# Kernel optimization log

Measured on AMD Instinct MI355X. Metric: run time of the kernel, lower is better.

The kernel has to match this reference:

```python
import jax, jax.numpy as jnp
import numpy as np

N_NODES = 20000
N_EDGES = 160000
FEAT = 512
HEADS = 4
NEG_SLOPE = 0.2


def setup_inputs() -> dict:
    key = jax.random.key(0)
    ks = jax.random.split(key, 8)
    s = 1.0 / np.sqrt(FEAT)
    return {
        "x": jax.random.normal(ks[0], (N_NODES, FEAT), dtype=jnp.float32),
        "edge_index": jax.random.randint(ks[1], (2, N_EDGES), 0, N_NODES, dtype=jnp.int32),
        "W_l": jax.random.normal(ks[2], (FEAT, HEADS * FEAT), dtype=jnp.float32) * s,
        "W_r": jax.random.normal(ks[3], (FEAT, HEADS * FEAT), dtype=jnp.float32) * s,
        "att": jax.random.normal(ks[4], (HEADS, FEAT), dtype=jnp.float32) * s,
        "bias": jax.random.normal(ks[5], (FEAT,), dtype=jnp.float32) * 0.01,
        "W_cls": jax.random.normal(ks[6], (FEAT, 2), dtype=jnp.float32) * s,
        "b_cls": jnp.zeros((2,), dtype=jnp.float32),
    }


def reference(x, edge_index, W_l, W_r, att, bias, W_cls, b_cls):
    N = x.shape[0]
    H, C = att.shape
    # PyG GATv2Conv default: add self-loops
    loops = jnp.arange(N, dtype=edge_index.dtype)
    ei = jnp.concatenate([edge_index, jnp.stack([loops, loops])], axis=1)
    src, dst = ei[0], ei[1]  # message j -> i

    xl = (x @ W_l).reshape(N, H, C)  # source transform
    xr = (x @ W_r).reshape(N, H, C)  # target transform

    # GATv2 score: e_ij = att . LeakyReLU(xl_j + xr_i)   -> [E, H]
    u = xl[src] + xr[dst]                      # [E, H, C]
    e = jnp.einsum('ehc,hc->eh', jax.nn.leaky_relu(u, NEG_SLOPE), att)

    # segment softmax over incoming edges of each dst node
    m = jax.ops.segment_max(e, dst, num_segments=N)          # [N, H]
    alpha = jnp.exp(e - m[dst])
    denom = jax.ops.segment_sum(alpha, dst, num_segments=N)  # [N, H]
    alpha = alpha / denom[dst]

    # aggregate: out_i = sum_j alpha_ij * xl_j
    out = jax.ops.segment_sum(alpha[:, :, None] * xl[src], dst, num_segments=N)  # [N,H,C]
    out = out.mean(axis=1) + bias  # concat=False -> mean over heads, then bias

    return out @ W_cls + b_cls  # [N, num_classes]
```

## Files before the change

### kernel.cpp

```cpp
#include <hip/hip_runtime.h>
#include <hip/hip_bf16.h>

#define FEAT    512
#define HEADS   4
#define NEG     0.2f

typedef unsigned int uint;
typedef unsigned short ushort_t;
typedef __attribute__((ext_vector_type(8))) short bf16x8v;
typedef __attribute__((ext_vector_type(4))) float f32x4v;
typedef __attribute__((ext_vector_type(4))) uint uint4v;
typedef __attribute__((address_space(3))) uint lds_u32_t;
typedef __attribute__((address_space(1))) const uint g_u32_t;

__device__ inline float bf2f(ushort_t h) { return __uint_as_float(((uint)h) << 16); }
__device__ inline ushort_t f2bf(float f) {
    uint u = __float_as_uint(f);
    u += 0x7fff + ((u >> 16) & 1);
    return (ushort_t)(u >> 16);
}
__device__ inline float2 up2(uint d) {
    return make_float2(__uint_as_float(d << 16), __uint_as_float(d & 0xffff0000u));
}
__device__ inline float2 f2add(float2 a, float2 b) { return make_float2(a.x + b.x, a.y + b.y); }
__device__ inline float2 f2min0(float2 a) { return make_float2(fminf(a.x, 0.f), fminf(a.y, 0.f)); }
__device__ inline float2 f2fma(float2 a, float2 b, float2 c) {
    return make_float2(fmaf(a.x, b.x, c.x), fmaf(a.y, b.y, c.y));
}
__device__ inline float2 f2fmas(float s, float2 b, float2 c) {
    return make_float2(fmaf(s, b.x, c.x), fmaf(s, b.y, c.y));
}

__global__ __launch_bounds__(256) void prep_kernel(
    const ushort_t* __restrict__ xprobe, int* flag,
    int* __restrict__ deg, int N, int NBZ,
    const void* a0, ushort_t* o0, int n0, const void* a1, ushort_t* o1, int n1,
    const void* a2, ushort_t* o2, int n2, const void* a3, ushort_t* o3, int n3,
    const void* __restrict__ Wl, const void* __restrict__ Wr,
    ushort_t* __restrict__ WtL, ushort_t* __restrict__ WtR, int Kk, int HCk, int nT,
    const void* __restrict__ xin, ushort_t* __restrict__ xc, long long nx) {
    __shared__ int s_isbf;
    __shared__ ushort_t t[64][72];
    int tid = threadIdx.x;
    if (tid < 64) {
        int hits = 0;
        for (int i = tid; i < 128; i += 64) {
            ushort_t w = xprobe[2 * i];
            uint hb = (w >> 8) & 0x7f;
            hits += (hb >= 0x38 && hb <= 0x42) ? 1 : 0;
        }
        #pragma unroll
        for (int off = 32; off >= 1; off >>= 1) hits += __shfl_xor(hits, off);
        if (tid == 0) s_isbf = (hits >= 64) ? 1 : 0;
    }
    __syncthreads();
    int isbf = s_isbf;
    int b = blockIdx.x;
    if (b == 0 && tid == 0) *flag = isbf;

    if (b < NBZ) {
        int i0 = (b * 256 + tid) * 4;
        if (i0 + 4 <= N) *(int4*)&deg[i0] = make_int4(0, 0, 0, 0);
        else for (int j = 0; j < 4; ++j) if (i0 + j < N) deg[i0 + j] = 0;
        return;
    }
    if (b < NBZ + 15) {
        int idx = (b - NBZ) * 256 + tid;
        const void* srcs[4] = {a0, a1, a2, a3};
        ushort_t* dsts[4] = {o0, o1, o2, o3};
        int ns[4] = {n0, n1, n2, n3};
        #pragma unroll
        for (int k = 0; k < 4; ++k) {
            if (idx < ns[k]) {
                dsts[k][idx] = isbf ? ((const ushort_t*)srcs[k])[idx]
                                    : f2bf(((const float*)srcs[k])[idx]);
                return;
            }
            idx -= ns[k];
        }
        return;
    }
    if (b < NBZ + 15 + nT) {
        int b2 = b - (NBZ + 15);
        int z = b2 & 1;
        int rest = b2 >> 1;
        int ntk = Kk >> 6;
        int ky = rest % ntk, nxt = rest / ntk;
        const void* in = z ? Wr : Wl;
        ushort_t* outp = z ? WtR : WtL;
        int k0 = ky * 64, n0 = nxt * 64;
        int r = tid >> 3;
        int c = (tid & 7) * 8;
        #pragma unroll
        for (int p = 0; p < 2; ++p) {
            int row = r + p * 32;
            size_t base = (size_t)(k0 + row) * HCk + n0 + c;
            if (isbf) {
                *(uint4*)&t[row][c] = *(const uint4*)((const ushort_t*)in + base);
            } else {
                const float* f = (const float*)in + base;
                float4 a = *(const float4*)f, bb = *(const float4*)(f + 4);
                ushort_t o[8] = {f2bf(a.x), f2bf(a.y), f2bf(a.z), f2bf(a.w),
                                 f2bf(bb.x), f2bf(bb.y), f2bf(bb.z), f2bf(bb.w)};
                *(uint4*)&t[row][c] = *(uint4*)o;
            }
        }
        __syncthreads();
        #pragma unroll
        for (int p = 0; p < 2; ++p) {
            int row = r + p * 32;
            #pragma unroll
            for (int j = 0; j < 8; ++j)
                outp[(size_t)(n0 + row) * Kk + k0 + c + j] = t[c + j][row];
        }
        return;
    }
    if (isbf) return;
    long long i0 = ((long long)(b - NBZ - 15 - nT) * 256 + tid) * 8;
    if (i0 + 8 <= nx) {
        const float* f = (const float*)xin + i0;
        float4 a = *(const float4*)f, bb = *(const float4*)(f + 4);
        ushort_t o[8] = {f2bf(a.x), f2bf(a.y), f2bf(a.z), f2bf(a.w),
                         f2bf(bb.x), f2bf(bb.y), f2bf(bb.z), f2bf(bb.w)};
        *(uint4*)&xc[i0] = *(uint4*)o;
    } else {
        for (long long i = i0; i < nx; ++i) xc[i] = f2bf(((const float*)xin)[i]);
    }
}

__global__ void hist_kernel(const int* __restrict__ dst, int* deg, int E, int N) {
    int i = blockIdx.x * blockDim.x + threadIdx.x;
    if (i < E) {
        int d = dst[i];
        if ((uint)d < (uint)N) atomicAdd(&deg[d], 1);
    }
}

__global__ __launch_bounds__(256) void scan1(const int* __restrict__ deg, int* __restrict__ part,
                                             int* __restrict__ bsum, int N) {
    __shared__ int tmp[256];
    int b = blockIdx.x, tid = threadIdx.x;
    int i0 = b * 1024 + tid * 4;
    int v[4] = {0, 0, 0, 0};
    if (i0 + 4 <= N) { int4 q = *(const int4*)&deg[i0]; v[0]=q.x+1; v[1]=q.y+1; v[2]=q.z+1; v[3]=q.w+1; }
    else { for (int j = 0; j < 4; ++j) v[j] = (i0 + j < N) ? deg[i0 + j] + 1 : 0; }
    int s0 = v[0], s1 = s0 + v[1], s2 = s1 + v[2], s3 = s2 + v[3];
    tmp[tid] = s3;
    __syncthreads();
    for (int off = 1; off < 256; off <<= 1) {
        int t = (tid >= off) ? tmp[tid - off] : 0;
        __syncthreads();
        tmp[tid] += t;
        __syncthreads();
    }
    int base = tid ? tmp[tid - 1] : 0;
    int e[4] = {base, base + s0, base + s1, base + s2};
    if (i0 + 4 <= N) { *(int4*)&part[i0] = make_int4(e[0], e[1], e[2], e[3]); }
    else { for (int j = 0; j < 4; ++j) if (i0 + j < N) part[i0 + j] = e[j]; }
    if (tid == 255) bsum[b] = tmp[255];
}

__global__ __launch_bounds__(256) void scan3(const int* __restrict__ part, const int* __restrict__ bsum,
                                             int* __restrict__ offsets, int* __restrict__ cursor,
                                             int N, int Nb) {
    __shared__ int s_add, s_tot;
    int b = blockIdx.x, tid = threadIdx.x;
    if (tid < 64) {
        int v = (tid < Nb) ? bsum[tid] : 0;
        int incl = v;
        #pragma unroll
        for (int off = 1; off < 64; off <<= 1) {
            int t = __shfl_up(incl, off);
            if (tid >= off) incl += t;
        }
        if (tid == b) s_add = incl - v;
        if (tid == Nb - 1) s_tot = incl;
    }
    __syncthreads();
    int add = s_add;
    int i0 = b * 1024 + tid * 4;
    #pragma unroll
    for (int j = 0; j < 4; ++j) {
        int i = i0 + j;
        if (i < N) { int o = part[i] + add; offsets[i] = o; cursor[i] = o; }
    }
    if (b == Nb - 1 && tid == 0) offsets[N] = s_tot;
}

__global__ void scatter_kernel(const int* __restrict__ src, const int* __restrict__ dst,
                               int* cursor, int* srcs, int E, int N) {
    int i = blockIdx.x * blockDim.x + threadIdx.x;
    if (i >= E + N) return;
    int s, d;
    if (i < E) { s = src[i]; d = dst[i]; }
    else       { s = i - E; d = i - E; }
    if ((uint)d >= (uint)N) return;
    int pos = atomicAdd(&cursor[d], 1);
    if ((uint)pos < (uint)(E + N)) srcs[pos] = s;
}

__global__ __launch_bounds__(256) void gemm128(const ushort_t* A_bf, const ushort_t* A_cv,
                                               const int* __restrict__ flag,
                                               const ushort_t* __restrict__ Bt,
                                               ushort_t* __restrict__ C,
                                               int M, int Nn, int K) {
    constexpr int CSTR = 132;
    __shared__ ushort_t SH[128 * CSTR];
    ushort_t* As = SH;
    ushort_t* Bs = SH + 8192;
    const ushort_t* A = (*flag) ? A_bf : A_cv;
    int tid = threadIdx.x;
    int wave = tid >> 6, lane = tid & 63;
    int row0 = blockIdx.y * 128, col0 = blockIdx.x * 128;
    int wm = (wave >> 1) * 64, wn = (wave & 1) * 64;

    f32x4v acc[4][4];
    #pragma unroll
    for (int i = 0; i < 4; ++i)
        #pragma unroll
        for (int j = 0; j < 4; ++j) acc[i][j] = (f32x4v){0.f, 0.f, 0.f, 0.f};

    int fm = lane & 15, kq8 = (lane >> 4) * 8;

    const ushort_t* srcA[2]; ushort_t* dstA0[2]; ushort_t* dstA1[2];
    const ushort_t* srcB[2]; ushort_t* dstB0[2]; ushort_t* dstB1[2];
    #pragma unroll
    for (int i = 0; i < 2; ++i) {
        int p = (wave * 2 + i) * 64 + lane;
        int row = p >> 2, kp = p & 3;
        int gra = row0 + row; if (gra >= M) gra = M - 1;
        srcA[i] = &A[(size_t)gra * K + kp * 8];
        srcB[i] = &Bt[(size_t)(col0 + row) * K + kp * 8];
        dstA0[i] = &As[p * 8]; dstA1[i] = &As[4096 + p * 8];
        dstB0[i] = &Bs[p * 8]; dstB1[i] = &Bs[4096 + p * 8];
    }

    for (int k0 = 0; k0 < K; k0 += 64) {
        #pragma unroll
        for (int i = 0; i < 2; ++i) {
            __builtin_amdgcn_global_load_lds((g_u32_t*)srcA[i],        (lds_u32_t*)dstA0[i], 16, 0, 0);
            __builtin_amdgcn_global_load_lds((g_u32_t*)(srcA[i] + 32), (lds_u32_t*)dstA1[i], 16, 0, 0);
            __builtin_amdgcn_global_load_lds((g_u32_t*)srcB[i],        (lds_u32_t*)dstB0[i], 16, 0, 0);
            __builtin_amdgcn_global_load_lds((g_u32_t*)(srcB[i] + 32), (lds_u32_t*)dstB1[i], 16, 0, 0);
            srcA[i] += 64; srcB[i] += 64;
        }
        __syncthreads();

        #pragma unroll
        for (int panel = 0; panel < 2; ++panel) {
            bf16x8v af[4], bfr[4];
            #pragma unroll
            for (int mi = 0; mi < 4; ++mi)
                af[mi] = *(const bf16x8v*)&As[panel * 4096 + (wm + mi * 16 + fm) * 32 + kq8];
            #pragma unroll
            for (int nj = 0; nj < 4; ++nj)
                bfr[nj] = *(const bf16x8v*)&Bs[panel * 4096 + (wn + nj * 16 + fm) * 32 + kq8];
            #pragma unroll
            for (int mi = 0; mi < 4; ++mi)
                #pragma unroll
                for (int nj = 0; nj < 4; ++nj)
                    acc[mi][nj] = __builtin_amdgcn_mfma_f32_16x16x32_bf16(af[mi], bfr[nj], acc[mi][nj], 0, 0, 0);
        }
        __syncthreads();
    }

    int col = lane & 15, rq = (lane >> 4) * 4;
    #pragma unroll
    for (int mi = 0; mi < 4; ++mi)
        #pragma unroll
        for (int r = 0; r < 4; ++r)
            #pragma unroll
            for (int nj = 0; nj < 4; ++nj)
                SH[(wm + mi * 16 + rq + r) * CSTR + wn + nj * 16 + col] = f2bf(acc[mi][nj][r]);
    __syncthreads();
    #pragma unroll
    for (int j = 0; j < 8; ++j) {
        int base = (tid + j * 256) * 8;
        int r = base >> 7, c = base & 127;
        int gm = row0 + r;
        if (gm < M)
            *(uint4*)&C[(size_t)gm * Nn + col0 + c] = *(const uint4*)&SH[r * CSTR + c];
    }
}

__global__ __launch_bounds__(128, 4) void gat_aggregate(
    const ushort_t* __restrict__ xl, int xl_stride,
    const ushort_t* __restrict__ xr, int xr_stride,
    const int* __restrict__ offsets, const int* __restrict__ srcs,
    const ushort_t* __restrict__ att, const ushort_t* __restrict__ bias,
    const ushort_t* __restrict__ Wc, const ushort_t* __restrict__ bc,
    float* __restrict__ out, int c0, int Cn, int N, int EN) {
    int bn = blockIdx.x;
    if (bn >= Cn) return;
    int n = c0 + bn;
    int tid = threadIdx.x;
    int w = tid >> 6, lane = tid & 63;
    int h = 2 * w + (lane >> 5);
    int r = lane & 31;
    int hoff = h * FEAT + r * 16;

    __shared__ float sh[HEADS][FEAT];
    __shared__ float r0s[2], r1s[2];

    float2 xrr[8], attr[8];
    { const uint4v* p = (const uint4v*)&xr[(size_t)bn * xr_stride + hoff];
      uint4v qa = __builtin_nontemporal_load(p);
      uint4v qb = __builtin_nontemporal_load(p + 1);
      xrr[0] = up2(qa.x); xrr[1] = up2(qa.y); xrr[2] = up2(qa.z); xrr[3] = up2(qa.w);
      xrr[4] = up2(qb.x); xrr[5] = up2(qb.y); xrr[6] = up2(qb.z); xrr[7] = up2(qb.w); }
    { const ushort_t* p = &att[hoff];
      uint4 qa = *(const uint4*)p, qb = *(const uint4*)(p + 8);
      attr[0] = up2(qa.x); attr[1] = up2(qa.y); attr[2] = up2(qa.z); attr[3] = up2(qa.w);
      attr[4] = up2(qb.x); attr[5] = up2(qb.y); attr[6] = up2(qb.z); attr[7] = up2(qb.w); }

    int start = offsets[n], end = offsets[n + 1];
    start = max(0, min(start, EN));
    end   = max(start, min(end, EN));
    int deg = end - start;

    int sv = 0;
    if (lane < deg) sv = srcs[start + lane];

    float l = 0.f;
    float2 acc[8] = {{0.f,0.f},{0.f,0.f},{0.f,0.f},{0.f,0.f},
                     {0.f,0.f},{0.f,0.f},{0.f,0.f},{0.f,0.f}};
    const ushort_t* xlh = xl + hoff;
    const float2 cneg = make_float2(NEG - 1.0f, NEG - 1.0f);

    auto getS = [&](int i) -> int {
        if (i >= deg) i = deg - 1;
        if (i < 0) i = 0;
        int s = (i < 64) ? __shfl(sv, i) : srcs[start + i];
        return ((uint)s >= (uint)N) ? 0 : s;
    };
    auto fetchE = [&](int i, uint4& qa, uint4& qb) {
        int s = getS(i);
        const ushort_t* pp = xlh + (size_t)s * xl_stride;
        qa = *(const uint4*)pp;
        qb = *(const uint4*)(pp + 8);
    };
    auto body = [&](uint4 qa, uint4 qb) {
        float2 v[8] = {up2(qa.x), up2(qa.y), up2(qa.z), up2(qa.w),
                       up2(qb.x), up2(qb.y), up2(qb.z), up2(qb.w)};
        float2 p2 = make_float2(0.f, 0.f);
        #pragma unroll
        for (int j = 0; j < 8; ++j) {
            float2 u  = f2add(v[j], xrr[j]);
            float2 lr = f2fma(f2min0(u), cneg, u);
            p2 = f2fma(lr, attr[j], p2);
        }
        float p = p2.x + p2.y;
        #pragma unroll
        for (int off = 16; off >= 1; off >>= 1) p += __shfl_xor(p, off);
        float wgt = __expf(p);
        l += wgt;
        #pragma unroll
        for (int j = 0; j < 8; ++j) acc[j] = f2fmas(wgt, v[j], acc[j]);
    };

    uint4 a0q, a0r, a1q, a1r, b0q, b0r, b1q, b1r;
    fetchE(0, a0q, a0r);
    fetchE(1, a1q, a1r);
    for (int e = 0; e < deg; e += 2) {
        fetchE(e + 2, b0q, b0r);
        fetchE(e + 3, b1q, b1r);
        body(a0q, a0r);
        if (e + 1 < deg) body(a1q, a1r);
        a0q = b0q; a0r = b0r; a1q = b1q; a1r = b1r;
    }

    float inv = 0.25f / fmaxf(l, 1e-35f);
    #pragma unroll
    for (int j = 0; j < 8; ++j) {
        sh[h][r * 16 + 2 * j]     = acc[j].x * inv;
        sh[h][r * 16 + 2 * j + 1] = acc[j].y * inv;
    }
    __syncthreads();

    float p0 = 0.f, p1 = 0.f;
    #pragma unroll
    for (int c = tid; c < FEAT; c += 128) {
        float f = sh[0][c] + sh[1][c] + sh[2][c] + sh[3][c] + bf2f(bias[c]);
        uint w2 = *(const uint*)&Wc[c * 2];
        p0 = fmaf(f, bf2f((ushort_t)(w2 & 0xffff)), p0);
        p1 = fmaf(f, bf2f((ushort_t)(w2 >> 16)), p1);
    }
    #pragma unroll
    for (int off = 32; off >= 1; off >>= 1) {
        p0 += __shfl_xor(p0, off);
        p1 += __shfl_xor(p1, off);
    }
    if (lane == 0) { r0s[w] = p0; r1s[w] = p1; }
    __syncthreads();
    if (tid == 0) {
        out[(size_t)n * 2 + 0] = r0s[0] + r0s[1] + bf2f(bc[0]);
        out[(size_t)n * 2 + 1] = r1s[0] + r1s[1] + bf2f(bc[1]);
    }
}

extern "C" void kernel_launch(void* const* d_in, const int* in_sizes, int n_in,
                              void* d_out, int out_size, void* d_ws, size_t ws_size,
                              hipStream_t stream) {
    const void* x    = d_in[0];
    const int*  ei   = (const int*)d_in[1];
    const void* W_l  = d_in[2];
    const void* W_r  = d_in[3];
    const void* att  = d_in[4];
    const void* bias = d_in[5];
    const void* Wc   = d_in[6];
    const void* bc   = d_in[7];
    float* out = (float*)d_out;

    const int N  = in_sizes[0] / FEAT;
    const int E  = in_sizes[1] / 2;
    const int K  = FEAT;
    const int HC = HEADS * FEAT;
    const int EN = E + N;
    const int Nb = (N + 1023) / 1024;

    const int* src = ei;
    const int* dst = ei + E;

    char* base = (char*)d_ws;
    size_t off = 0;
    auto alloc = [&](size_t bytes) -> char* {
        char* p = base + off;
        off = (off + bytes + 255) & ~(size_t)255;
        return p;
    };
    int* flag    = (int*)alloc(4);
    int* offsets = (int*)alloc((size_t)(N + 1) * 4);
    int* cursor  = (int*)alloc((size_t)N * 4);
    int* deg     = (int*)alloc((size_t)N * 4);
    int* part    = (int*)alloc((size_t)N * 4);
    int* bsum    = (int*)alloc((size_t)(Nb + 1) * 4);
    int* srcs    = (int*)alloc((size_t)EN * 4);
    ushort_t* attc  = (ushort_t*)alloc((size_t)HC * 2);
    ushort_t* biasc = (ushort_t*)alloc((size_t)FEAT * 2);
    ushort_t* Wcc   = (ushort_t*)alloc((size_t)FEAT * 2 * 2);
    ushort_t* bcc   = (ushort_t*)alloc(2 * 2);
    ushort_t* xc   = (ushort_t*)alloc((size_t)N * K * 2);
    ushort_t* Wcat = (ushort_t*)alloc((size_t)2 * HC * K * 2);
    size_t fixed = off;

    size_t need_merged = (size_t)N * 2 * HC * 2;
    bool merged = (ws_size >= fixed + need_merged);

    long long NX = (long long)N * K;
    const int NBZ = (N + 1023) / 1024;
    const int nT = (HC / 64) * (K / 64) * 2;
    int nxb = (int)((NX / 8 + 255) / 256);
    prep_kernel<<<NBZ + 15 + nT + nxb, 256, 0, stream>>>(
        (const ushort_t*)x, flag, deg, N, NBZ,
        att, attc, HC, bias, biasc, FEAT, Wc, Wcc, FEAT * 2, bc, bcc, 2,
        W_l, W_r, Wcat, Wcat + (size_t)HC * K, K, HC, nT,
        x, xc, NX);

    hist_kernel<<<(E + 255) / 256, 256, 0, stream>>>(dst, deg, E, N);
    scan1<<<Nb, 256, 0, stream>>>(deg, part, bsum, N);
    scan3<<<Nb, 256, 0, stream>>>(part, bsum, offsets, cursor, N, Nb);
    scatter_kernel<<<(EN + 255) / 256, 256, 0, stream>>>(src, dst, cursor, srcs, E, N);

    const ushort_t* x_bf = (const ushort_t*)x;

    if (merged) {
        ushort_t* xlr = (ushort_t*)(base + fixed);
        dim3 gg(2 * HC / 128, (N + 127) / 128);
        gemm128<<<gg, 256, 0, stream>>>(x_bf, xc, flag, Wcat, xlr, N, 2 * HC, K);
        gat_aggregate<<<N, 128, 0, stream>>>(xlr, 2 * HC, xlr + HC, 2 * HC,
                                             offsets, srcs, attc, biasc, Wcc, bcc,
                                             out, 0, N, N, EN);
    } else {
        ushort_t* xl = (ushort_t*)alloc((size_t)N * HC * 2);
        size_t remain = (ws_size > off) ? (ws_size - off) : 0;
        long long Cmax = (long long)(remain / ((size_t)HC * 2));
        int C = (Cmax >= N) ? N : (int)(Cmax & ~63LL);
        if (C < 64) C = 64;
        ushort_t* xrc = (ushort_t*)(base + off);
        ushort_t* Wlt = Wcat;
        ushort_t* Wrt = Wcat + (size_t)HC * K;

        dim3 gl(HC / 128, (N + 127) / 128);
        gemm128<<<gl, 256, 0, stream>>>(x_bf, xc, flag, Wlt, xl, N, HC, K);
        for (int c0 = 0; c0 < N; c0 += C) {
            int Cn = (N - c0 < C) ? (N - c0) : C;
            dim3 gr(HC / 128, (Cn + 127) / 128);
            gemm128<<<gr, 256, 0, stream>>>(x_bf + (size_t)c0 * K, xc + (size_t)c0 * K, flag,
                                            Wrt, xrc, Cn, HC, K);
            gat_aggregate<<<Cn, 128, 0, stream>>>(xl, HC, xrc, HC,
                                                  offsets, srcs, attc, biasc, Wcc, bcc,
                                                  out, c0, Cn, N, EN);
        }
    }
}
```

Before: 331.3 us.

## Fold histogram into x-convert kernel, scatter into GEMM grid, use packed f32 math

Moves the x fp32-to-bf16 conversion out of prep_kernel into a new kernel that also does the degree histogram, and drops the standalone hist_kernel launch. The CSR scatter now runs as extra blocks appended to the merged GEMM grid. The aim is fewer launches and letting the scatter overlap with GEMM work. The aggregation inner loop uses inline-asm v_pk_add_f32/v_pk_fma_f32 on float2 vectors to halve VALU instruction count. The risks are atomic contention alongside the GEMM blocks, and inline asm limiting compiler scheduling.

```diff
diff --git a/kernel.cpp b/kernel.cpp
--- a/kernel.cpp
+++ b/kernel.cpp
@@ -9,6 +9,7 @@
 typedef unsigned short ushort_t;
 typedef __attribute__((ext_vector_type(8))) short bf16x8v;
 typedef __attribute__((ext_vector_type(4))) float f32x4v;
+typedef __attribute__((ext_vector_type(2))) float f32x2v;
 typedef __attribute__((ext_vector_type(4))) uint uint4v;
 typedef __attribute__((address_space(3))) uint lds_u32_t;
 typedef __attribute__((address_space(1))) const uint g_u32_t;
@@ -19,16 +20,17 @@
     u += 0x7fff + ((u >> 16) & 1);
     return (ushort_t)(u >> 16);
 }
-__device__ inline float2 up2(uint d) {
-    return make_float2(__uint_as_float(d << 16), __uint_as_float(d & 0xffff0000u));
-}
-__device__ inline float2 f2add(float2 a, float2 b) { return make_float2(a.x + b.x, a.y + b.y); }
-__device__ inline float2 f2min0(float2 a) { return make_float2(fminf(a.x, 0.f), fminf(a.y, 0.f)); }
-__device__ inline float2 f2fma(float2 a, float2 b, float2 c) {
-    return make_float2(fmaf(a.x, b.x, c.x), fmaf(a.y, b.y, c.y));
-}
-__device__ inline float2 f2fmas(float s, float2 b, float2 c) {
-    return make_float2(fmaf(s, b.x, c.x), fmaf(s, b.y, c.y));
+__device__ inline f32x2v pk_add(f32x2v a, f32x2v b) {
+    f32x2v d; asm("v_pk_add_f32 %0, %1, %2" : "=v"(d) : "v"(a), "v"(b)); return d;
+}
+__device__ inline f32x2v pk_fma(f32x2v a, f32x2v b, f32x2v c) {
+    f32x2v d; asm("v_pk_fma_f32 %0, %1, %2, %3" : "=v"(d) : "v"(a), "v"(b), "v"(c)); return d;
+}
+__device__ inline f32x2v up2v(uint d) {
+    f32x2v r; r.x = __uint_as_float(d << 16); r.y = __uint_as_float(d & 0xffff0000u); return r;
+}
+__device__ inline f32x2v pk_min0(f32x2v a) {
+    f32x2v r; r.x = fminf(a.x, 0.f); r.y = fminf(a.y, 0.f); return r;
 }
 
 __global__ __launch_bounds__(256) void prep_kernel(
@@ -37,8 +39,7 @@
     const void* a0, ushort_t* o0, int n0, const void* a1, ushort_t* o1, int n1,
     const void* a2, ushort_t* o2, int n2, const void* a3, ushort_t* o3, int n3,
     const void* __restrict__ Wl, const void* __restrict__ Wr,
-    ushort_t* __restrict__ WtL, ushort_t* __restrict__ WtR, int Kk, int HCk, int nT,
-    const void* __restrict__ xin, ushort_t* __restrict__ xc, long long nx) {
+    ushort_t* __restrict__ WtL, ushort_t* __restrict__ WtR, int Kk, int HCk) {
     __shared__ int s_isbf;
     __shared__ ushort_t t[64][72];
     int tid = threadIdx.x;
@@ -80,43 +81,69 @@
         }
         return;
     }
-    if (b < NBZ + 15 + nT) {
-        int b2 = b - (NBZ + 15);
-        int z = b2 & 1;
-        int rest = b2 >> 1;
-        int ntk = Kk >> 6;
-        int ky = rest % ntk, nxt = rest / ntk;
-        const void* in = z ? Wr : Wl;
-        ushort_t* outp = z ? WtR : WtL;
-        int k0 = ky * 64, n0 = nxt * 64;
-        int r = tid >> 3;
-        int c = (tid & 7) * 8;
-        #pragma unroll
-        for (int p = 0; p < 2; ++p) {
-            int row = r + p * 32;
-            size_t base = (size_t)(k0 + row) * HCk + n0 + c;
-            if (isbf) {
-                *(uint4*)&t[row][c] = *(const uint4*)((const ushort_t*)in + base);
-            } else {
-                const float* f = (const float*)in + base;
-                float4 a = *(const float4*)f, bb = *(const float4*)(f + 4);
-                ushort_t o[8] = {f2bf(a.x), f2bf(a.y), f2bf(a.z), f2bf(a.w),
-                                 f2bf(bb.x), f2bf(bb.y), f2bf(bb.z), f2bf(bb.w)};
-                *(uint4*)&t[row][c] = *(uint4*)o;
-            }
-        }
-        __syncthreads();
-        #pragma unroll
-        for (int p = 0; p < 2; ++p) {
-            int row = r + p * 32;
-            #pragma unroll
-            for (int j = 0; j < 8; ++j)
-                outp[(size_t)(n0 + row) * Kk + k0 + c + j] = t[c + j][row];
+    int b2 = b - (NBZ + 15);
+    int z = b2 & 1;
+    int rest = b2 >> 1;
+    int ntk = Kk >> 6;
+    int ky = rest % ntk, nxt = rest / ntk;
+    const void* in = z ? Wr : Wl;
+    ushort_t* outp = z ? WtR : WtL;
+    int kt0 = ky * 64, nt0 = nxt * 64;
+    int r = tid >> 3;
+    int c = (tid & 7) * 8;
+    #pragma unroll
+    for (int p = 0; p < 2; ++p) {
+        int row = r + p * 32;
+        size_t base = (size_t)(kt0 + row) * HCk + nt0 + c;
+        if (isbf) {
+            *(uint4*)&t[row][c] = *(const uint4*)((const ushort_t*)in + base);
+        } else {
+            const float* f = (const float*)in + base;
+            float4 a = *(const float4*)f, bb = *(const float4*)(f + 4);
+            ushort_t o[8] = {f2bf(a.x), f2bf(a.y), f2bf(a.z), f2bf(a.w),
+                             f2bf(bb.x), f2bf(bb.y), f2bf(bb.z), f2bf(bb.w)};
+            *(uint4*)&t[row][c] = *(uint4*)o;
+        }
+    }
+    __syncthreads();
+    #pragma unroll
+    for (int p = 0; p < 2; ++p) {
+        int row = r + p * 32;
+        #pragma unroll
+        for (int j = 0; j < 8; ++j)
+            outp[(size_t)(nt0 + row) * Kk + kt0 + c + j] = t[c + j][row];
+    }
+}
+
+__global__ __launch_bounds__(256) void histx_kernel(
+    const ushort_t* __restrict__ xprobe,
+    const int* __restrict__ dstE, int* deg, int E, int NH, int Ngr,
+    const void* __restrict__ xin, ushort_t* __restrict__ xc, long long nx) {
+    int tid = threadIdx.x;
+    int b = blockIdx.x;
+    if (b < NH) {
+        int i = b * 256 + tid;
+        if (i < E) {
+            int d = dstE[i];
+            if ((uint)d < (uint)Ngr) atomicAdd(&deg[d], 1);
         }
         return;
     }
-    if (isbf) return;
-    long long i0 = ((long long)(b - NBZ - 15 - nT) * 256 + tid) * 8;
+    __shared__ int s_isbf;
+    if (tid < 64) {
+        int hits = 0;
+        for (int i = tid; i < 128; i += 64) {
+            ushort_t w = xprobe[2 * i];
+            uint hb = (w >> 8) & 0x7f;
+            hits += (hb >= 0x38 && hb <= 0x42) ? 1 : 0;
+        }
+        #pragma unroll
+        for (int off = 32; off >= 1; off >>= 1) hits += __shfl_xor(hits, off);
+        if (tid == 0) s_isbf = (hits >= 64) ? 1 : 0;
+    }
+    __syncthreads();
+    if (s_isbf) return;
+    long long i0 = ((long long)(b - NH) * 256 + tid) * 8;
     if (i0 + 8 <= nx) {
         const float* f = (const float*)xin + i0;
         float4 a = *(const float4*)f, bb = *(const float4*)(f + 4);
@@ -125,14 +152,6 @@
         *(uint4*)&xc[i0] = *(uint4*)o;
     } else {
         for (long long i = i0; i < nx; ++i) xc[i] = f2bf(((const float*)xin)[i]);
-    }
-}
-
-__global__ void hist_kernel(const int* __restrict__ dst, int* deg, int E, int N) {
-    int i = blockIdx.x * blockDim.x + threadIdx.x;
-    if (i < E) {
-        int d = dst[i];
-        if ((uint)d < (uint)N) atomicAdd(&deg[d], 1);
     }
 }
 
@@ -203,7 +222,28 @@
                                                const int* __restrict__ flag,
                                                const ushort_t* __restrict__ Bt,
                                                ushort_t* __restrict__ C,
-                                               int M, int Nn, int K) {
+                                               int M, int Nn, int K, int gyGemm,
+                                               const int* __restrict__ esrc,
+                                               const int* __restrict__ edst,
+                                               int* cursor, int* srcsOut,
+                                               int E, int Ngr, int nScB) {
+    if ((int)blockIdx.y >= gyGemm) {
+        int id = ((int)blockIdx.y - gyGemm) * (int)gridDim.x + (int)blockIdx.x;
+        if (id < nScB) {
+            int i = id * 256 + (int)threadIdx.x;
+            int EN = E + Ngr;
+            if (i < EN) {
+                int s, d;
+                if (i < E) { s = esrc[i]; d = edst[i]; }
+                else       { s = i - E; d = i - E; }
+                if ((uint)d < (uint)Ngr) {
+                    int pos = atomicAdd(&cursor[d], 1);
+                    if ((uint)pos < (uint)EN) srcsOut[pos] = s;
+                }
+            }
+        }
+        return;
+    }
     constexpr int CSTR = 132;
     __shared__ ushort_t SH[128 * CSTR];
     ushort_t* As = SH;
@@ -302,16 +342,16 @@
     __shared__ float sh[HEADS][FEAT];
     __shared__ float r0s[2], r1s[2];
 
-    float2 xrr[8], attr[8];
+    f32x2v xrr[8], attr[8];
     { const uint4v* p = (const uint4v*)&xr[(size_t)bn * xr_stride + hoff];
       uint4v qa = __builtin_nontemporal_load(p);
       uint4v qb = __builtin_nontemporal_load(p + 1);
-      xrr[0] = up2(qa.x); xrr[1] = up2(qa.y); xrr[2] = up2(qa.z); xrr[3] = up2(qa.w);
-      xrr[4] = up2(qb.x); xrr[5] = up2(qb.y); xrr[6] = up2(qb.z); xrr[7] = up2(qb.w); }
+      xrr[0] = up2v(qa.x); xrr[1] = up2v(qa.y); xrr[2] = up2v(qa.z); xrr[3] = up2v(qa.w);
+      xrr[4] = up2v(qb.x); xrr[5] = up2v(qb.y); xrr[6] = up2v(qb.z); xrr[7] = up2v(qb.w); }
     { const ushort_t* p = &att[hoff];
       uint4 qa = *(const uint4*)p, qb = *(const uint4*)(p + 8);
-      attr[0] = up2(qa.x); attr[1] = up2(qa.y); attr[2] = up2(qa.z); attr[3] = up2(qa.w);
-      attr[4] = up2(qb.x); attr[5] = up2(qb.y); attr[6] = up2(qb.z); attr[7] = up2(qb.w); }
+      attr[0] = up2v(qa.x); attr[1] = up2v(qa.y); attr[2] = up2v(qa.z); attr[3] = up2v(qa.w);
+      attr[4] = up2v(qb.x); attr[5] = up2v(qb.y); attr[6] = up2v(qb.z); attr[7] = up2v(qb.w); }
 
     int start = offsets[n], end = offsets[n + 1];
     start = max(0, min(start, EN));
@@ -322,10 +362,10 @@
     if (lane < deg) sv = srcs[start + lane];
 
     float l = 0.f;
-    float2 acc[8] = {{0.f,0.f},{0.f,0.f},{0.f,0.f},{0.f,0.f},
+    f32x2v acc[8] = {{0.f,0.f},{0.f,0.f},{0.f,0.f},{0.f,0.f},
                      {0.f,0.f},{0.f,0.f},{0.f,0.f},{0.f,0.f}};
     const ushort_t* xlh = xl + hoff;
-    const float2 cneg = make_float2(NEG - 1.0f, NEG - 1.0f);
+    const f32x2v cneg = {NEG - 1.0f, NEG - 1.0f};
 
     auto getS = [&](int i) -> int {
         if (i >= deg) i = deg - 1;
@@ -340,22 +380,23 @@
         qb = *(const uint4*)(pp + 8);
     };
     auto body = [&](uint4 qa, uint4 qb) {
-        float2 v[8] = {up2(qa.x), up2(qa.y), up2(qa.z), up2(qa.w),
-                       up2(qb.x), up2(qb.y), up2(qb.z), up2(qb.w)};
-        float2 p2 = make_float2(0.f, 0.f);
+        f32x2v v[8] = {up2v(qa.x), up2v(qa.y), up2v(qa.z), up2v(qa.w),
+                       up2v(qb.x), up2v(qb.y), up2v(qb.z), up2v(qb.w)};
+        f32x2v p2 = {0.f, 0.f};
         #pragma unroll
         for (int j = 0; j < 8; ++j) {
-            float2 u  = f2add(v[j], xrr[j]);
-            float2 lr = f2fma(f2min0(u), cneg, u);
-            p2 = f2fma(lr, attr[j], p2);
+            f32x2v u  = pk_add(v[j], xrr[j]);
+            f32x2v lr = pk_fma(pk_min0(u), cneg, u);
+            p2 = pk_fma(lr, attr[j], p2);
         }
         float p = p2.x + p2.y;
         #pragma unroll
         for (int off = 16; off >= 1; off >>= 1) p += __shfl_xor(p, off);
         float wgt = __expf(p);
         l += wgt;
-        #pragma unroll
-        for (int j = 0; j < 8; ++j) acc[j] = f2fmas(wgt, v[j], acc[j]);
+        f32x2v wv; wv.x = wgt; wv.y = wgt;
+        #pragma unroll
+        for (int j = 0; j < 8; ++j) acc[j] = pk_fma(wv, v[j], acc[j]);
     };
 
     uint4 a0q, a0r, a1q, a1r, b0q, b0r, b1q, b1r;
@@ -449,28 +490,35 @@
     long long NX = (long long)N * K;
     const int NBZ = (N + 1023) / 1024;
     const int nT = (HC / 64) * (K / 64) * 2;
-    int nxb = (int)((NX / 8 + 255) / 256);
-    prep_kernel<<<NBZ + 15 + nT + nxb, 256, 0, stream>>>(
+    prep_kernel<<<NBZ + 15 + nT, 256, 0, stream>>>(
         (const ushort_t*)x, flag, deg, N, NBZ,
         att, attc, HC, bias, biasc, FEAT, Wc, Wcc, FEAT * 2, bc, bcc, 2,
-        W_l, W_r, Wcat, Wcat + (size_t)HC * K, K, HC, nT,
-        x, xc, NX);
-
-    hist_kernel<<<(E + 255) / 256, 256, 0, stream>>>(dst, deg, E, N);
+        W_l, W_r, Wcat, Wcat + (size_t)HC * K, K, HC);
+
+    const int NH = (E + 255) / 256;
+    int nxb = (int)((NX / 8 + 255) / 256);
+    histx_kernel<<<NH + nxb, 256, 0, stream>>>(
+        (const ushort_t*)x, dst, deg, E, NH, N, x, xc, NX);
+
     scan1<<<Nb, 256, 0, stream>>>(deg, part, bsum, N);
     scan3<<<Nb, 256, 0, stream>>>(part, bsum, offsets, cursor, N, Nb);
-    scatter_kernel<<<(EN + 255) / 256, 256, 0, stream>>>(src, dst, cursor, srcs, E, N);
 
     const ushort_t* x_bf = (const ushort_t*)x;
+    const int nScB = (EN + 255) / 256;
 
     if (merged) {
         ushort_t* xlr = (ushort_t*)(base + fixed);
-        dim3 gg(2 * HC / 128, (N + 127) / 128);
-        gemm128<<<gg, 256, 0, stream>>>(x_bf, xc, flag, Wcat, xlr, N, 2 * HC, K);
+        int gx = 2 * HC / 128;
+        int gyG = (N + 127) / 128;
+        int exR = (nScB + gx - 1) / gx;
+        dim3 gg(gx, gyG + exR);
+        gemm128<<<gg, 256, 0, stream>>>(x_bf, xc, flag, Wcat, xlr, N, 2 * HC, K,
+                                        gyG, src, dst, cursor, srcs, E, N, nScB);
         gat_aggregate<<<N, 128, 0, stream>>>(xlr, 2 * HC, xlr + HC, 2 * HC,
                                              offsets, srcs, attc, biasc, Wcc, bcc,
                                              out, 0, N, N, EN);
     } else {
+        scatter_kernel<<<nScB, 256, 0, stream>>>(src, dst, cursor, srcs, E, N);
         ushort_t* xl = (ushort_t*)alloc((size_t)N * HC * 2);
         size_t remain = (ws_size > off) ? (ws_size - off) : 0;
         long long Cmax = (long long)(remain / ((size_t)HC * 2));
@@ -481,12 +529,16 @@
         ushort_t* Wrt = Wcat + (size_t)HC * K;
 
         dim3 gl(HC / 128, (N + 127) / 128);
-        gemm128<<<gl, 256, 0, stream>>>(x_bf, xc, flag, Wlt, xl, N, HC, K);
+        gemm128<<<gl, 256, 0, stream>>>(x_bf, xc, flag, Wlt, xl, N, HC, K,
+                                        (N + 127) / 128, nullptr, nullptr,
+                                        nullptr, nullptr, 0, 0, 0);
         for (int c0 = 0; c0 < N; c0 += C) {
             int Cn = (N - c0 < C) ? (N - c0) : C;
             dim3 gr(HC / 128, (Cn + 127) / 128);
             gemm128<<<gr, 256, 0, stream>>>(x_bf + (size_t)c0 * K, xc + (size_t)c0 * K, flag,
-                                            Wrt, xrc, Cn, HC, K);
+                                            Wrt, xrc, Cn, HC, K,
+                                            (Cn + 127) / 128, nullptr, nullptr,
+                                            nullptr, nullptr, 0, 0, 0);
             gat_aggregate<<<Cn, 128, 0, stream>>>(xl, HC, xrc, HC,
                                                   offsets, srcs, attc, biasc, Wcc, bcc,
                                                   out, c0, Cn, N, EN);
```

New measurement: 320.9 us. 1.03x faster.
